# Kernel optimization log

Measured on AMD Instinct MI355X. Metric: run time of the kernel, lower is better.

## Reference

```python
import math
import jax, jax.numpy as jnp
import numpy as np

B, CH3, T = 64, 192, 2048  # B = batch*heads, CH3 = 3*head_dim

def setup_inputs() -> dict:
    key = jax.random.key(0)
    qkv = jax.random.normal(key, (B, CH3, T), dtype=jnp.float32)
    return {"qkv": qkv}

def reference(qkv):
    ch = qkv.shape[1] // 3
    q, k, v = jnp.split(qkv, 3, axis=1)  # each [B, ch, T]
    scale = 1.0 / math.sqrt(math.sqrt(ch))
    # scores [B, T(query), S(key)]
    weight = jnp.einsum('bct,bcs->bts', q * scale, k * scale)
    weight = jax.nn.softmax(weight.astype(jnp.float32), axis=-1).astype(weight.dtype)
    return jnp.einsum('bts,bcs->bct', weight, v)
```

## Files before the change

kernel.cpp:

```cpp
#include <hip/hip_runtime.h>


#define DHEAD 64
#define TLEN  2048
#define NB    64
#define BQ    256
#define BK    64
#define LDA   72
#define LDT   65

typedef _Float16 h16x8 __attribute__((ext_vector_type(8)));
typedef _Float16 h16x4 __attribute__((ext_vector_type(4)));
typedef _Float16 h16x2 __attribute__((ext_vector_type(2)));
typedef __fp16   fp16x2 __attribute__((ext_vector_type(2)));
typedef float f32x4 __attribute__((ext_vector_type(4)));

#define QK_SCALE 0.35355339059327373f

__device__ __forceinline__ h16x2 pkrtz(float a, float b) {
    union { fp16x2 f; h16x2 h; } u;
    u.f = __builtin_amdgcn_cvt_pkrtz(a, b);
    return u.h;
}

__global__ __launch_bounds__(256)
void prep_qk(const float* __restrict__ qkv, _Float16* __restrict__ ws) {
    __shared__ float T32[64 * LDT];
    const int tile = blockIdx.x, tensor = blockIdx.y, b = blockIdx.z;
    const int tid = threadIdx.x;
    const float* src = qkv + ((size_t)b * 3 + tensor) * DHEAD * TLEN + tile * 64;
    _Float16* dst = ws + (size_t)tensor * NB * DHEAD * TLEN
                  + (size_t)b * DHEAD * TLEN + (size_t)tile * 64 * DHEAD;
    {
        int c = tid >> 4, t4 = (tid & 15) * 4;
        #pragma unroll
        for (int rr = 0; rr < 4; ++rr, c += 16) {
            float4 f = *(const float4*)(src + c * TLEN + t4);
            T32[(t4 + 0) * LDT + c] = f.x;
            T32[(t4 + 1) * LDT + c] = f.y;
            T32[(t4 + 2) * LDT + c] = f.z;
            T32[(t4 + 3) * LDT + c] = f.w;
        }
    }
    __syncthreads();
    #pragma unroll
    for (int rep = 0; rep < 2; ++rep) {
        int idx = rep * 256 + tid;
        int t = idx >> 3, j = idx & 7;
        const float* row = &T32[t * LDT + j * 8];
        union { h16x8 v; h16x2 h[4]; } o;
        o.h[0] = pkrtz(row[0] * QK_SCALE, row[1] * QK_SCALE);
        o.h[1] = pkrtz(row[2] * QK_SCALE, row[3] * QK_SCALE);
        o.h[2] = pkrtz(row[4] * QK_SCALE, row[5] * QK_SCALE);
        o.h[3] = pkrtz(row[6] * QK_SCALE, row[7] * QK_SCALE);
        *(h16x8*)(dst + t * DHEAD + j * 8) = o.v;
    }
}

__global__ __launch_bounds__(256)
void prep_v(const float* __restrict__ qkv, _Float16* __restrict__ ws) {
    const int tile = blockIdx.x, b = blockIdx.y;
    const int tid = threadIdx.x;
    const float* src = qkv + ((size_t)b * 3 + 2) * DHEAD * TLEN + tile * 256;
    _Float16* dst = ws + (size_t)2 * NB * DHEAD * TLEN
                  + (size_t)b * DHEAD * TLEN + tile * 256;
    int c = tid >> 5, t8 = (tid & 31) * 8;
    #pragma unroll
    for (int rr = 0; rr < 8; ++rr, c += 8) {
        float4 f0 = *(const float4*)(src + c * TLEN + t8);
        float4 f1 = *(const float4*)(src + c * TLEN + t8 + 4);
        union { h16x8 v; h16x2 h[4]; } o;
        o.h[0] = pkrtz(f0.x, f0.y);
        o.h[1] = pkrtz(f0.z, f0.w);
        o.h[2] = pkrtz(f1.x, f1.y);
        o.h[3] = pkrtz(f1.z, f1.w);
        *(h16x8*)(dst + c * TLEN + t8) = o.v;
    }
}

__global__ __launch_bounds__(256, 2)
void attn(const _Float16* __restrict__ ws, float* __restrict__ out) {
    __shared__ alignas(16) _Float16 Ks[64 * LDA];
    __shared__ alignas(16) _Float16 Vs[64 * LDA];
    __shared__ alignas(16) _Float16 Pt[4][64 * LDA];

    const int tid  = threadIdx.x;
    const int wave = tid >> 6;
    const int lane = tid & 63;
    const int quad = lane >> 4;
    const int c16  = lane & 15;

    const int b  = blockIdx.y;
    const int t0 = blockIdx.x * BQ;

    const _Float16* qt = ws + (size_t)b * DHEAD * TLEN + (size_t)(t0 + wave * 64) * DHEAD;
    const _Float16* kt = ws + (size_t)NB * DHEAD * TLEN + (size_t)b * DHEAD * TLEN;
    const _Float16* vd = ws + (size_t)2 * NB * DHEAD * TLEN + (size_t)b * DHEAD * TLEN;

    h16x8 qf[4][2];
    #pragma unroll
    for (int ts = 0; ts < 4; ++ts)
        #pragma unroll
        for (int kk = 0; kk < 2; ++kk)
            qf[ts][kk] = *(const h16x8*)(qt + (size_t)(ts * 16 + c16) * DHEAD + kk * 32 + quad * 8);

    f32x4 acco[4][4];
    #pragma unroll
    for (int i = 0; i < 4; ++i)
        #pragma unroll
        for (int j = 0; j < 4; ++j) acco[i][j] = f32x4{0.f, 0.f, 0.f, 0.f};
    float lp[4] = {0.f, 0.f, 0.f, 0.f};

    _Float16* Pw = Pt[wave];

    h16x8 kc[2], vc[2];
    #pragma unroll
    for (int r = 0; r < 2; ++r) {
        int id = tid + r * 256;
        kc[r] = *(const h16x8*)(kt + (size_t)id * 8);
        vc[r] = *(const h16x8*)(vd + (size_t)(id >> 3) * TLEN + (id & 7) * 8);
    }

    for (int it = 0; it < TLEN / BK; ++it) {
        __syncthreads();
        #pragma unroll
        for (int r = 0; r < 2; ++r) {
            int id = tid + r * 256;
            *(h16x8*)(&Ks[(id >> 3) * LDA + (id & 7) * 8]) = kc[r];
            *(h16x8*)(&Vs[(id >> 3) * LDA + (id & 7) * 8]) = vc[r];
        }
        __syncthreads();

        if (it + 1 < TLEN / BK) {
            int s0 = (it + 1) * BK;
            #pragma unroll
            for (int r = 0; r < 2; ++r) {
                int id = tid + r * 256;
                kc[r] = *(const h16x8*)(kt + (size_t)s0 * DHEAD + id * 8);
                vc[r] = *(const h16x8*)(vd + (size_t)(id >> 3) * TLEN + s0 + (id & 7) * 8);
            }
        }

        f32x4 accs[4][4];
        #pragma unroll
        for (int i = 0; i < 4; ++i)
            #pragma unroll
            for (int j = 0; j < 4; ++j) accs[i][j] = f32x4{0.f, 0.f, 0.f, 0.f};
        #pragma unroll
        for (int kk = 0; kk < 2; ++kk)
            #pragma unroll
            for (int st = 0; st < 4; ++st) {
                h16x8 ka = *(const h16x8*)(&Ks[(st * 16 + c16) * LDA + kk * 32 + quad * 8]);
                #pragma unroll
                for (int ts = 0; ts < 4; ++ts)
                    accs[st][ts] = __builtin_amdgcn_mfma_f32_16x16x32_f16(ka, qf[ts][kk], accs[st][ts], 0, 0, 0);
            }

        #pragma unroll
        for (int st = 0; st < 4; ++st)
            #pragma unroll
            for (int ts = 0; ts < 4; ++ts) {
                f32x4 v = accs[st][ts];
                float e0 = __expf(v[0]);
                float e1 = __expf(v[1]);
                float e2 = __expf(v[2]);
                float e3 = __expf(v[3]);
                lp[ts] += (e0 + e1) + (e2 + e3);
                union { h16x4 v4; h16x2 h[2]; } p;
                p.h[0] = pkrtz(e0, e1);
                p.h[1] = pkrtz(e2, e3);
                *(h16x4*)(&Pw[(ts * 16 + c16) * LDA + st * 16 + quad * 4]) = p.v4;
            }

        #pragma unroll
        for (int kk = 0; kk < 2; ++kk) {
            h16x8 pb[4];
            #pragma unroll
            for (int ts = 0; ts < 4; ++ts)
                pb[ts] = *(const h16x8*)(&Pw[(ts * 16 + c16) * LDA + kk * 32 + quad * 8]);
            #pragma unroll
            for (int cst = 0; cst < 4; ++cst) {
                h16x8 va = *(const h16x8*)(&Vs[(cst * 16 + c16) * LDA + kk * 32 + quad * 8]);
                #pragma unroll
                for (int ts = 0; ts < 4; ++ts)
                    acco[cst][ts] = __builtin_amdgcn_mfma_f32_16x16x32_f16(va, pb[ts], acco[cst][ts], 0, 0, 0);
            }
        }
    }

    float rinv[4];
    #pragma unroll
    for (int ts = 0; ts < 4; ++ts) {
        float l = lp[ts];
        l += __shfl_xor(l, 16);
        l += __shfl_xor(l, 32);
        rinv[ts] = 1.0f / l;
    }

    float* ob = out + (size_t)b * DHEAD * TLEN + t0 + wave * 64;
    #pragma unroll
    for (int cst = 0; cst < 4; ++cst)
        #pragma unroll
        for (int ts = 0; ts < 4; ++ts)
            #pragma unroll
            for (int r = 0; r < 4; ++r)
                ob[(size_t)(cst * 16 + quad * 4 + r) * TLEN + ts * 16 + c16] = acco[cst][ts][r] * rinv[ts];
}

extern "C" void kernel_launch(void* const* d_in, const int* in_sizes, int n_in,
                              void* d_out, int out_size, void* d_ws, size_t ws_size,
                              hipStream_t stream) {
    const float* qkv = (const float*)d_in[0];
    _Float16* ws = (_Float16*)d_ws;
    float* out = (float*)d_out;
    prep_qk<<<dim3(TLEN / 64, 2, NB), 256, 0, stream>>>(qkv, ws);
    prep_v<<<dim3(TLEN / 256, NB), 256, 0, stream>>>(qkv, ws);
    attn<<<dim3(TLEN / BQ, NB), 256, 0, stream>>>(ws, out);
}
```

Baseline: 241.7 us.

## Halve query tile, swizzle LDS, use exp2 scaling, merge prep kernels

The query block per workgroup drops from 256 to 128 rows, giving 32 rows per wave, and launch bounds rise to 4 blocks per CU to improve occupancy and fill more CUs (1024 blocks instead of 512). Padded LDS rows are replaced with an XOR-swizzled 64-wide layout, which reduces shared memory use and avoids bank conflicts. The Q/K scale is folded with log2(e) so the softmax can use the native exp2 instruction. The two prep kernels are merged into a single launch. In exchange, each K/V tile is reused across fewer query rows, which increases LDS and L2 traffic per unit of output.

```diff
diff --git a/kernel.cpp b/kernel.cpp
--- a/kernel.cpp
+++ b/kernel.cpp
@@ -4,9 +4,8 @@
 #define DHEAD 64
 #define TLEN  2048
 #define NB    64
-#define BQ    256
+#define BQ    128
 #define BK    64
-#define LDA   72
 #define LDT   65
 
 typedef _Float16 h16x8 __attribute__((ext_vector_type(8)));
@@ -15,7 +14,9 @@
 typedef __fp16   fp16x2 __attribute__((ext_vector_type(2)));
 typedef float f32x4 __attribute__((ext_vector_type(4)));
 
-#define QK_SCALE 0.35355339059327373f
+#define QK_SCALE 0.42466090267246895f
+
+extern "C" __device__ float __ocml_native_exp2_f32(float);
 
 __device__ __forceinline__ h16x2 pkrtz(float a, float b) {
     union { fp16x2 f; h16x2 h; } u;
@@ -23,66 +24,70 @@
     return u.h;
 }
 
+__device__ __forceinline__ int swz(int row, int col) {
+    return row * 64 + (col ^ ((row & 7) << 3));
+}
+
 __global__ __launch_bounds__(256)
-void prep_qk(const float* __restrict__ qkv, _Float16* __restrict__ ws) {
+void prep(const float* __restrict__ qkv, _Float16* __restrict__ ws) {
     __shared__ float T32[64 * LDT];
-    const int tile = blockIdx.x, tensor = blockIdx.y, b = blockIdx.z;
+    const int bx = blockIdx.x, b = blockIdx.y;
     const int tid = threadIdx.x;
-    const float* src = qkv + ((size_t)b * 3 + tensor) * DHEAD * TLEN + tile * 64;
-    _Float16* dst = ws + (size_t)tensor * NB * DHEAD * TLEN
-                  + (size_t)b * DHEAD * TLEN + (size_t)tile * 64 * DHEAD;
-    {
-        int c = tid >> 4, t4 = (tid & 15) * 4;
-        #pragma unroll
-        for (int rr = 0; rr < 4; ++rr, c += 16) {
-            float4 f = *(const float4*)(src + c * TLEN + t4);
-            T32[(t4 + 0) * LDT + c] = f.x;
-            T32[(t4 + 1) * LDT + c] = f.y;
-            T32[(t4 + 2) * LDT + c] = f.z;
-            T32[(t4 + 3) * LDT + c] = f.w;
-        }
-    }
-    __syncthreads();
-    #pragma unroll
-    for (int rep = 0; rep < 2; ++rep) {
-        int idx = rep * 256 + tid;
-        int t = idx >> 3, j = idx & 7;
-        const float* row = &T32[t * LDT + j * 8];
-        union { h16x8 v; h16x2 h[4]; } o;
-        o.h[0] = pkrtz(row[0] * QK_SCALE, row[1] * QK_SCALE);
-        o.h[1] = pkrtz(row[2] * QK_SCALE, row[3] * QK_SCALE);
-        o.h[2] = pkrtz(row[4] * QK_SCALE, row[5] * QK_SCALE);
-        o.h[3] = pkrtz(row[6] * QK_SCALE, row[7] * QK_SCALE);
-        *(h16x8*)(dst + t * DHEAD + j * 8) = o.v;
-    }
-}
-
-__global__ __launch_bounds__(256)
-void prep_v(const float* __restrict__ qkv, _Float16* __restrict__ ws) {
-    const int tile = blockIdx.x, b = blockIdx.y;
-    const int tid = threadIdx.x;
-    const float* src = qkv + ((size_t)b * 3 + 2) * DHEAD * TLEN + tile * 256;
-    _Float16* dst = ws + (size_t)2 * NB * DHEAD * TLEN
-                  + (size_t)b * DHEAD * TLEN + tile * 256;
-    int c = tid >> 5, t8 = (tid & 31) * 8;
-    #pragma unroll
-    for (int rr = 0; rr < 8; ++rr, c += 8) {
-        float4 f0 = *(const float4*)(src + c * TLEN + t8);
-        float4 f1 = *(const float4*)(src + c * TLEN + t8 + 4);
-        union { h16x8 v; h16x2 h[4]; } o;
-        o.h[0] = pkrtz(f0.x, f0.y);
-        o.h[1] = pkrtz(f0.z, f0.w);
-        o.h[2] = pkrtz(f1.x, f1.y);
-        o.h[3] = pkrtz(f1.z, f1.w);
-        *(h16x8*)(dst + c * TLEN + t8) = o.v;
-    }
-}
-
-__global__ __launch_bounds__(256, 2)
+
+    if (bx < 64) {
+        const int tensor = bx >> 5, tile = bx & 31;
+        const float* src = qkv + ((size_t)b * 3 + tensor) * DHEAD * TLEN + tile * 64;
+        _Float16* dst = ws + (size_t)tensor * NB * DHEAD * TLEN
+                      + (size_t)b * DHEAD * TLEN + (size_t)tile * 64 * DHEAD;
+        {
+            int c = tid >> 4, t4 = (tid & 15) * 4;
+            #pragma unroll
+            for (int rr = 0; rr < 4; ++rr, c += 16) {
+                float4 f = *(const float4*)(src + c * TLEN + t4);
+                T32[(t4 + 0) * LDT + c] = f.x;
+                T32[(t4 + 1) * LDT + c] = f.y;
+                T32[(t4 + 2) * LDT + c] = f.z;
+                T32[(t4 + 3) * LDT + c] = f.w;
+            }
+        }
+        __syncthreads();
+        #pragma unroll
+        for (int rep = 0; rep < 2; ++rep) {
+            int idx = rep * 256 + tid;
+            int t = idx >> 3, j = idx & 7;
+            const float* row = &T32[t * LDT + j * 8];
+            union { h16x8 v; h16x2 h[4]; } o;
+            o.h[0] = pkrtz(row[0] * QK_SCALE, row[1] * QK_SCALE);
+            o.h[1] = pkrtz(row[2] * QK_SCALE, row[3] * QK_SCALE);
+            o.h[2] = pkrtz(row[4] * QK_SCALE, row[5] * QK_SCALE);
+            o.h[3] = pkrtz(row[6] * QK_SCALE, row[7] * QK_SCALE);
+            *(h16x8*)(dst + t * DHEAD + j * 8) = o.v;
+        }
+    } else {
+        const int tile = bx - 64;
+        const float* src = qkv + ((size_t)b * 3 + 2) * DHEAD * TLEN + tile * 64;
+        _Float16* dst = ws + (size_t)2 * NB * DHEAD * TLEN
+                      + (size_t)b * DHEAD * TLEN + tile * 64;
+        int c = tid >> 3, t8 = (tid & 7) * 8;
+        #pragma unroll
+        for (int rr = 0; rr < 2; ++rr, c += 32) {
+            float4 f0 = *(const float4*)(src + c * TLEN + t8);
+            float4 f1 = *(const float4*)(src + c * TLEN + t8 + 4);
+            union { h16x8 v; h16x2 h[4]; } o;
+            o.h[0] = pkrtz(f0.x, f0.y);
+            o.h[1] = pkrtz(f0.z, f0.w);
+            o.h[2] = pkrtz(f1.x, f1.y);
+            o.h[3] = pkrtz(f1.z, f1.w);
+            *(h16x8*)(dst + c * TLEN + t8) = o.v;
+        }
+    }
+}
+
+__global__ __launch_bounds__(256, 4)
 void attn(const _Float16* __restrict__ ws, float* __restrict__ out) {
-    __shared__ alignas(16) _Float16 Ks[64 * LDA];
-    __shared__ alignas(16) _Float16 Vs[64 * LDA];
-    __shared__ alignas(16) _Float16 Pt[4][64 * LDA];
+    __shared__ alignas(16) _Float16 Ks[64 * 64];
+    __shared__ alignas(16) _Float16 Vs[64 * 64];
+    __shared__ alignas(16) _Float16 Pt[4][32 * 64];
 
     const int tid  = threadIdx.x;
     const int wave = tid >> 6;
@@ -93,23 +98,23 @@
     const int b  = blockIdx.y;
     const int t0 = blockIdx.x * BQ;
 
-    const _Float16* qt = ws + (size_t)b * DHEAD * TLEN + (size_t)(t0 + wave * 64) * DHEAD;
+    const _Float16* qt = ws + (size_t)b * DHEAD * TLEN + (size_t)(t0 + wave * 32) * DHEAD;
     const _Float16* kt = ws + (size_t)NB * DHEAD * TLEN + (size_t)b * DHEAD * TLEN;
     const _Float16* vd = ws + (size_t)2 * NB * DHEAD * TLEN + (size_t)b * DHEAD * TLEN;
 
-    h16x8 qf[4][2];
-    #pragma unroll
-    for (int ts = 0; ts < 4; ++ts)
+    h16x8 qf[2][2];
+    #pragma unroll
+    for (int ts = 0; ts < 2; ++ts)
         #pragma unroll
         for (int kk = 0; kk < 2; ++kk)
             qf[ts][kk] = *(const h16x8*)(qt + (size_t)(ts * 16 + c16) * DHEAD + kk * 32 + quad * 8);
 
-    f32x4 acco[4][4];
+    f32x4 acco[4][2];
     #pragma unroll
     for (int i = 0; i < 4; ++i)
         #pragma unroll
-        for (int j = 0; j < 4; ++j) acco[i][j] = f32x4{0.f, 0.f, 0.f, 0.f};
-    float lp[4] = {0.f, 0.f, 0.f, 0.f};
+        for (int j = 0; j < 2; ++j) acco[i][j] = f32x4{0.f, 0.f, 0.f, 0.f};
+    float lp[2] = {0.f, 0.f};
 
     _Float16* Pw = Pt[wave];
 
@@ -126,8 +131,9 @@
         #pragma unroll
         for (int r = 0; r < 2; ++r) {
             int id = tid + r * 256;
-            *(h16x8*)(&Ks[(id >> 3) * LDA + (id & 7) * 8]) = kc[r];
-            *(h16x8*)(&Vs[(id >> 3) * LDA + (id & 7) * 8]) = vc[r];
+            int row = id >> 3, col = (id & 7) * 8;
+            *(h16x8*)(&Ks[swz(row, col)]) = kc[r];
+            *(h16x8*)(&Vs[swz(row, col)]) = vc[r];
         }
         __syncthreads();
 
@@ -141,67 +147,67 @@
             }
         }
 
-        f32x4 accs[4][4];
+        f32x4 accs[4][2];
         #pragma unroll
         for (int i = 0; i < 4; ++i)
             #pragma unroll
-            for (int j = 0; j < 4; ++j) accs[i][j] = f32x4{0.f, 0.f, 0.f, 0.f};
+            for (int j = 0; j < 2; ++j) accs[i][j] = f32x4{0.f, 0.f, 0.f, 0.f};
         #pragma unroll
         for (int kk = 0; kk < 2; ++kk)
             #pragma unroll
             for (int st = 0; st < 4; ++st) {
-                h16x8 ka = *(const h16x8*)(&Ks[(st * 16 + c16) * LDA + kk * 32 + quad * 8]);
+                h16x8 ka = *(const h16x8*)(&Ks[swz(st * 16 + c16, kk * 32 + quad * 8)]);
                 #pragma unroll
-                for (int ts = 0; ts < 4; ++ts)
+                for (int ts = 0; ts < 2; ++ts)
                     accs[st][ts] = __builtin_amdgcn_mfma_f32_16x16x32_f16(ka, qf[ts][kk], accs[st][ts], 0, 0, 0);
             }
 
         #pragma unroll
         for (int st = 0; st < 4; ++st)
             #pragma unroll
-            for (int ts = 0; ts < 4; ++ts) {
+            for (int ts = 0; ts < 2; ++ts) {
                 f32x4 v = accs[st][ts];
-                float e0 = __expf(v[0]);
-                float e1 = __expf(v[1]);
-                float e2 = __expf(v[2]);
-                float e3 = __expf(v[3]);
+                float e0 = __ocml_native_exp2_f32(v[0]);
+                float e1 = __ocml_native_exp2_f32(v[1]);
+                float e2 = __ocml_native_exp2_f32(v[2]);
+                float e3 = __ocml_native_exp2_f32(v[3]);
                 lp[ts] += (e0 + e1) + (e2 + e3);
                 union { h16x4 v4; h16x2 h[2]; } p;
                 p.h[0] = pkrtz(e0, e1);
                 p.h[1] = pkrtz(e2, e3);
-                *(h16x4*)(&Pw[(ts * 16 + c16) * LDA + st * 16 + quad * 4]) = p.v4;
+                *(h16x4*)(&Pw[swz(ts * 16 + c16, st * 16 + quad * 4)]) = p.v4;
             }
 
         #pragma unroll
         for (int kk = 0; kk < 2; ++kk) {
-            h16x8 pb[4];
-            #pragma unroll
-            for (int ts = 0; ts < 4; ++ts)
-                pb[ts] = *(const h16x8*)(&Pw[(ts * 16 + c16) * LDA + kk * 32 + quad * 8]);
+            h16x8 pb[2];
+            #pragma unroll
+            for (int ts = 0; ts < 2; ++ts)
+                pb[ts] = *(const h16x8*)(&Pw[swz(ts * 16 + c16, kk * 32 + quad * 8)]);
             #pragma unroll
             for (int cst = 0; cst < 4; ++cst) {
-                h16x8 va = *(const h16x8*)(&Vs[(cst * 16 + c16) * LDA + kk * 32 + quad * 8]);
+                h16x8 va = *(const h16x8*)(&Vs[swz(cst * 16 + c16, kk * 32 + quad * 8)]);
                 #pragma unroll
-                for (int ts = 0; ts < 4; ++ts)
+                for (int ts = 0; ts < 2; ++ts)
                     acco[cst][ts] = __builtin_amdgcn_mfma_f32_16x16x32_f16(va, pb[ts], acco[cst][ts], 0, 0, 0);
             }
         }
     }
 
-    float rinv[4];
-    #pragma unroll
-    for (int ts = 0; ts < 4; ++ts) {
+    float rinv[2];
+    #pragma unroll
+    for (int ts = 0; ts < 2; ++ts) {
         float l = lp[ts];
         l += __shfl_xor(l, 16);
         l += __shfl_xor(l, 32);
         rinv[ts] = 1.0f / l;
     }
 
-    float* ob = out + (size_t)b * DHEAD * TLEN + t0 + wave * 64;
+    float* ob = out + (size_t)b * DHEAD * TLEN + t0 + wave * 32;
     #pragma unroll
     for (int cst = 0; cst < 4; ++cst)
         #pragma unroll
-        for (int ts = 0; ts < 4; ++ts)
+        for (int ts = 0; ts < 2; ++ts)
             #pragma unroll
             for (int r = 0; r < 4; ++r)
                 ob[(size_t)(cst * 16 + quad * 4 + r) * TLEN + ts * 16 + c16] = acco[cst][ts][r] * rinv[ts];
@@ -213,7 +219,6 @@
     const float* qkv = (const float*)d_in[0];
     _Float16* ws = (_Float16*)d_ws;
     float* out = (float*)d_out;
-    prep_qk<<<dim3(TLEN / 64, 2, NB), 256, 0, stream>>>(qkv, ws);
-    prep_v<<<dim3(TLEN / 256, NB), 256, 0, stream>>>(qkv, ws);
+    prep<<<dim3(96, NB), 256, 0, stream>>>(qkv, ws);
     attn<<<dim3(TLEN / BQ, NB), 256, 0, stream>>>(ws, out);
 }
```

New measurement: 239.8 us. No clear change (-0.8%).
